# Optimization experiments

Hardware: AMD Instinct MI355X
Metric: run time of the kernel (lower is better)

## Reference

```python
import jax, jax.numpy as jnp
import numpy as np

H, T, E = 8, 2048, 512


def setup_inputs() -> dict:
    key = jax.random.key(0)
    ks = jax.random.split(key, 11)
    s_e = 1.0 / np.sqrt(E)
    s_f = 1.0 / np.sqrt(H * T)
    return {
        "x": jax.random.normal(ks[0], (T, E), jnp.float32),
        "y": jax.random.normal(ks[1], (T, E), jnp.float32),
        "z": jax.random.normal(ks[2], (T, E), jnp.float32),
        "Wq": jax.random.normal(ks[3], (H, E, E), jnp.float32) * s_e,
        "bq": jax.random.normal(ks[4], (H, E), jnp.float32) * s_e,
        "Wk": jax.random.normal(ks[5], (H, E, E), jnp.float32) * s_e,
        "bk": jax.random.normal(ks[6], (H, E), jnp.float32) * s_e,
        "Wv": jax.random.normal(ks[7], (H, E, E), jnp.float32) * s_e,
        "bv": jax.random.normal(ks[8], (H, E), jnp.float32) * s_e,
        "Wf": jax.random.normal(ks[9], (T, H * T), jnp.float32) * s_f,
        "bf": jax.random.normal(ks[10], (T,), jnp.float32) * s_f,
    }


def reference(x, y, z, Wq, bq, Wk, bk, Wv, bv, Wf, bf):
    # Per-head projections: torch Linear is x @ W.T + b, W is [out,in]
    q = jnp.einsum("se,hfe->hsf", x, Wq) + bq[:, None, :]  # [H,T,E]
    k = jnp.einsum("se,hfe->hsf", y, Wk) + bk[:, None, :]
    v = jnp.einsum("se,hfe->hsf", z, Wv) + bv[:, None, :]
    # Scores scaled by sqrt(num query rows) = sqrt(T), as in the source
    scores = jnp.einsum("hsf,htf->hst", q, k) / jnp.sqrt(jnp.asarray(T, x.dtype))
    att = jax.nn.softmax(scores, axis=-1)
    heads_out = jnp.einsum("hst,htf->hsf", att, v)  # [H,T,E]
    concat = heads_out.reshape(H * T, E)  # cat along dim 0
    # finalLinear applied to concat.T: [E, H*T] @ Wf.T -> [E, T], then transpose
    final = (concat.T @ Wf.T + bf).T  # [T, E]
    residual = final + z
    # Manual per-row LayerNorm: (x - mean) / sqrt(std^2 + 1e-4), population std
    mean = jnp.mean(residual, axis=1, keepdims=True)
    var = jnp.var(residual, axis=1, keepdims=True)
    return (residual - mean) / jnp.sqrt(var + 1e-4)
```

## Files before the change

kernel.cpp:

```cpp
#include <hip/hip_runtime.h>
#include <hip/hip_bf16.h>
#include <cstdint>


#define HH 8
#define TT 2048
#define EE 512
#define HT (HH * TT)
#define HE (HH * EE)

typedef __bf16 bf16_t;
typedef __attribute__((ext_vector_type(8))) __bf16 bf16x8;
typedef __attribute__((ext_vector_type(4))) float f32x4;

__device__ __forceinline__ void stage_half(const bf16_t* __restrict__ g, bf16_t* l) {
  __builtin_amdgcn_global_load_lds(
      (const __attribute__((address_space(1))) unsigned int*)g,
      (__attribute__((address_space(3))) unsigned int*)l, 16, 0, 0);
}
__device__ __forceinline__ void stage_half(const float* __restrict__ g, bf16_t* l) {
  float4 u = ((const float4*)g)[0];
  float4 v = ((const float4*)g)[1];
  bf16x8 o;
  o[0] = (__bf16)u.x; o[1] = (__bf16)u.y; o[2] = (__bf16)u.z; o[3] = (__bf16)u.w;
  o[4] = (__bf16)v.x; o[5] = (__bf16)v.y; o[6] = (__bf16)v.z; o[7] = (__bf16)v.w;
  *(bf16x8*)l = o;
}

template <typename AT, typename CT>
__global__ __launch_bounds__(256) void mfma_gemm_nt(
    const AT* __restrict__ A, const bf16_t* __restrict__ B, CT* __restrict__ C,
    const float* __restrict__ bias_m, const float* __restrict__ bias_n,
    int K, int lda, int ldb, int ldc,
    int64_t sA, int64_t sB, int64_t sC, int64_t sBM, int64_t sBN) {
  const int gx = gridDim.x, gy = gridDim.y;
  const int nwg = gx * gy * (int)gridDim.z;
  const int lin = blockIdx.x + gx * (blockIdx.y + gy * blockIdx.z);
  const int qn = nwg >> 3, rn = nwg & 7;
  const int xcd = lin & 7, sub = lin >> 3;
  const int wgid = (xcd < rn ? xcd * (qn + 1) : rn * (qn + 1) + (xcd - rn) * qn) + sub;
  const int bx = wgid % gx;
  const int t1 = wgid / gx;
  const int by = t1 % gy;
  const int z = t1 / gy;

  A += z * sA;
  B += z * sB;
  C += z * sC;
  if (bias_m) bias_m += z * sBM;
  if (bias_n) bias_n += z * sBN;

  const int m0 = bx * 128;
  const int n0 = by * 128;
  const int tid = threadIdx.x;

  __shared__ bf16_t sAb[128 * 32];
  __shared__ bf16_t sBb[128 * 32];

  const int srow = tid >> 2;
  const int scol = (tid & 3) * 8;
  const AT* a0 = A + (int64_t)(m0 + srow) * lda + scol;
  const AT* a1 = a0 + (int64_t)64 * lda;
  const bf16_t* b0 = B + (int64_t)(n0 + srow) * ldb + scol;
  const bf16_t* b1 = b0 + (int64_t)64 * ldb;
  bf16_t* la0 = sAb + tid * 8;
  bf16_t* la1 = sAb + 2048 + tid * 8;
  bf16_t* lb0 = sBb + tid * 8;
  bf16_t* lb1 = sBb + 2048 + tid * 8;

  const int wave = tid >> 6;
  const int lane = tid & 63;
  const int wm = (wave >> 1) * 64;
  const int wn = (wave & 1) * 64;
  const int fr = lane & 15;
  const int qd = lane >> 4;

  f32x4 acc[4][4];
#pragma unroll
  for (int i = 0; i < 4; i++)
#pragma unroll
    for (int j = 0; j < 4; j++) acc[i][j] = (f32x4){0.f, 0.f, 0.f, 0.f};

  for (int kt = 0; kt < K; kt += 32) {
    __syncthreads();
    stage_half(a0 + kt, la0);
    stage_half(a1 + kt, la1);
    stage_half(b0 + kt, lb0);
    stage_half(b1 + kt, lb1);
    __syncthreads();

    bf16x8 af[4], bf_[4];
#pragma unroll
    for (int i = 0; i < 4; i++)
      af[i] = *(const bf16x8*)&sAb[(wm + i * 16 + fr) * 32 + qd * 8];
#pragma unroll
    for (int j = 0; j < 4; j++)
      bf_[j] = *(const bf16x8*)&sBb[(wn + j * 16 + fr) * 32 + qd * 8];
#pragma unroll
    for (int i = 0; i < 4; i++)
#pragma unroll
      for (int j = 0; j < 4; j++)
        acc[i][j] = __builtin_amdgcn_mfma_f32_16x16x32_bf16(af[i], bf_[j], acc[i][j], 0, 0, 0);
  }

#pragma unroll
  for (int i = 0; i < 4; i++) {
    const int row0 = m0 + wm + i * 16 + qd * 4;
#pragma unroll
    for (int j = 0; j < 4; j++) {
      const int col = n0 + wn + j * 16 + fr;
      const float bn = bias_n ? bias_n[col] : 0.f;
#pragma unroll
      for (int r = 0; r < 4; r++) {
        const float bm = bias_m ? bias_m[row0 + r] : 0.f;
        C[(int64_t)(row0 + r) * ldc + col] = (CT)(acc[i][j][r] + bn + bm);
      }
    }
  }
}

__global__ __launch_bounds__(256) void cvt_bf16(const float* __restrict__ s,
                                                bf16_t* __restrict__ d) {
  const int64_t i = ((int64_t)blockIdx.x * 256 + threadIdx.x) * 8;
  float4 u = ((const float4*)(s + i))[0];
  float4 v = ((const float4*)(s + i))[1];
  bf16x8 o;
  o[0] = (__bf16)u.x; o[1] = (__bf16)u.y; o[2] = (__bf16)u.z; o[3] = (__bf16)u.w;
  o[4] = (__bf16)v.x; o[5] = (__bf16)v.y; o[6] = (__bf16)v.z; o[7] = (__bf16)v.w;
  *(bf16x8*)(d + i) = o;
}

__global__ __launch_bounds__(256) void softmax_rows(bf16_t* __restrict__ S) {
  const float scale = 0.022097086912079608f;
  bf16_t* p = S + (int64_t)blockIdx.x * TT;
  const int tid = threadIdx.x;
  bf16x8 in = *(const bf16x8*)(p + tid * 8);
  float v[8];
  float mx = -1e30f;
#pragma unroll
  for (int i = 0; i < 8; i++) {
    v[i] = (float)in[i] * scale;
    mx = fmaxf(mx, v[i]);
  }
#pragma unroll
  for (int o = 32; o > 0; o >>= 1) mx = fmaxf(mx, __shfl_xor(mx, o));
  __shared__ float redm[4], reds[4];
  if ((tid & 63) == 0) redm[tid >> 6] = mx;
  __syncthreads();
  mx = fmaxf(fmaxf(redm[0], redm[1]), fmaxf(redm[2], redm[3]));
  float sum = 0.f;
#pragma unroll
  for (int i = 0; i < 8; i++) {
    v[i] = __expf(v[i] - mx);
    sum += v[i];
  }
#pragma unroll
  for (int o = 32; o > 0; o >>= 1) sum += __shfl_xor(sum, o);
  if ((tid & 63) == 0) reds[tid >> 6] = sum;
  __syncthreads();
  sum = reds[0] + reds[1] + reds[2] + reds[3];
  const float inv = 1.0f / sum;
  bf16x8 o8;
#pragma unroll
  for (int i = 0; i < 8; i++) o8[i] = (__bf16)(v[i] * inv);
  *(bf16x8*)(p + tid * 8) = o8;
}

__global__ __launch_bounds__(256) void ln_res(const float* __restrict__ F,
                                              const float* __restrict__ Z,
                                              const float* __restrict__ BF,
                                              float* __restrict__ O) {
  const int row = blockIdx.x;
  const int tid = threadIdx.x;
  const int64_t off = (int64_t)row * EE + tid;
  float a = 0.f, b = 0.f;
#pragma unroll
  for (int pz = 0; pz < 8; pz++) {
    const float* f = F + (int64_t)pz * TT * EE;
    a += f[off];
    b += f[off + 256];
  }
  const float bft = BF[row];
  a += bft + Z[off];
  b += bft + Z[off + 256];
  float s = a + b, ss = a * a + b * b;
#pragma unroll
  for (int w = 32; w > 0; w >>= 1) {
    s += __shfl_xor(s, w);
    ss += __shfl_xor(ss, w);
  }
  __shared__ float rs[4], rss[4];
  if ((tid & 63) == 0) {
    rs[tid >> 6] = s;
    rss[tid >> 6] = ss;
  }
  __syncthreads();
  s = rs[0] + rs[1] + rs[2] + rs[3];
  ss = rss[0] + rss[1] + rss[2] + rss[3];
  const float mean = s * (1.0f / EE);
  const float var = ss * (1.0f / EE) - mean * mean;
  const float inv = rsqrtf(var + 1e-4f);
  float* o = O + (int64_t)row * EE;
  o[tid] = (a - mean) * inv;
  o[tid + 256] = (b - mean) * inv;
}

extern "C" void kernel_launch(void* const* d_in, const int* in_sizes, int n_in,
                              void* d_out, int out_size, void* d_ws, size_t ws_size,
                              hipStream_t stream) {
  const float* x = (const float*)d_in[0];
  const float* y = (const float*)d_in[1];
  const float* z = (const float*)d_in[2];
  const float* Wq = (const float*)d_in[3];
  const float* bq = (const float*)d_in[4];
  const float* Wk = (const float*)d_in[5];
  const float* bk = (const float*)d_in[6];
  const float* Wv = (const float*)d_in[7];
  const float* bv = (const float*)d_in[8];
  const float* Wf = (const float*)d_in[9];
  const float* bfb = (const float*)d_in[10];
  float* out = (float*)d_out;

  const size_t MB = 1ull << 20;
  char* p = (char*)d_ws;

  const int64_t nTE = (int64_t)TT * EE;
  const int64_t nW = (int64_t)HH * EE * EE;

  if (ws_size >= 151 * MB) {
    bf16_t* xb = (bf16_t*)(p + 0 * MB);
    bf16_t* yb = (bf16_t*)(p + 2 * MB);
    bf16_t* zb = (bf16_t*)(p + 4 * MB);
    bf16_t* Wqb = (bf16_t*)(p + 6 * MB);
    bf16_t* Wkb = (bf16_t*)(p + 10 * MB);
    bf16_t* Wvb = (bf16_t*)(p + 14 * MB);
    bf16_t* q = (bf16_t*)(p + 18 * MB);
    bf16_t* k = (bf16_t*)(p + 34 * MB);
    bf16_t* vT = (bf16_t*)(p + 50 * MB);
    bf16_t* att = (bf16_t*)(p + 66 * MB);
    bf16_t* hoT = (bf16_t*)(p + 130 * MB);
    float* finp = (float*)(p + 18 * MB);

    cvt_bf16<<<nTE / 2048, 256, 0, stream>>>(x, xb);
    cvt_bf16<<<nTE / 2048, 256, 0, stream>>>(y, yb);
    cvt_bf16<<<nTE / 2048, 256, 0, stream>>>(z, zb);
    cvt_bf16<<<nW / 2048, 256, 0, stream>>>(Wq, Wqb);
    cvt_bf16<<<nW / 2048, 256, 0, stream>>>(Wk, Wkb);
    cvt_bf16<<<nW / 2048, 256, 0, stream>>>(Wv, Wvb);

    mfma_gemm_nt<bf16_t, bf16_t><<<dim3(16, 32, 1), 256, 0, stream>>>(
        xb, Wqb, q, nullptr, bq, EE, EE, EE, HE, 0, 0, 0, 0, 0);
    mfma_gemm_nt<bf16_t, bf16_t><<<dim3(16, 32, 1), 256, 0, stream>>>(
        yb, Wkb, k, nullptr, bk, EE, EE, EE, HE, 0, 0, 0, 0, 0);
    mfma_gemm_nt<bf16_t, bf16_t><<<dim3(32, 16, 1), 256, 0, stream>>>(
        Wvb, zb, vT, bv, nullptr, EE, EE, EE, TT, 0, 0, 0, 0, 0);
    mfma_gemm_nt<bf16_t, bf16_t><<<dim3(16, 16, 8), 256, 0, stream>>>(
        q, k, att, nullptr, nullptr, EE, HE, HE, TT, EE, EE, (int64_t)TT * TT, 0, 0);
    softmax_rows<<<HH * TT, 256, 0, stream>>>(att);
    mfma_gemm_nt<bf16_t, bf16_t><<<dim3(4, 16, 8), 256, 0, stream>>>(
        vT, att, hoT, nullptr, nullptr, TT, TT, TT, HT, (int64_t)EE * TT, (int64_t)TT * TT,
        (int64_t)TT, 0, 0);
    mfma_gemm_nt<float, float><<<dim3(16, 4, 8), 256, 0, stream>>>(
        Wf, hoT, finp, nullptr, nullptr, HT / 8, HT, HT, EE, HT / 8, HT / 8,
        (int64_t)TT * EE, 0, 0);
    ln_res<<<TT, 256, 0, stream>>>(finp, z, bfb, out);
  } else {
    bf16_t* xb = (bf16_t*)(p + 0 * MB);
    bf16_t* yb = (bf16_t*)(p + 2 * MB);
    bf16_t* zb = (bf16_t*)(p + 4 * MB);
    bf16_t* Wqb = (bf16_t*)(p + 6 * MB);
    bf16_t* Wkb = (bf16_t*)(p + 10 * MB);
    bf16_t* Wvb = (bf16_t*)(p + 14 * MB);
    bf16_t* qh = (bf16_t*)(p + 18 * MB);
    bf16_t* kh = (bf16_t*)(p + 20 * MB);
    bf16_t* vTh = (bf16_t*)(p + 22 * MB);
    bf16_t* att = (bf16_t*)(p + 24 * MB);
    bf16_t* hoT = (bf16_t*)(p + 32 * MB);
    float* finp = (float*)(p + 0 * MB);

    cvt_bf16<<<nTE / 2048, 256, 0, stream>>>(x, xb);
    cvt_bf16<<<nTE / 2048, 256, 0, stream>>>(y, yb);
    cvt_bf16<<<nTE / 2048, 256, 0, stream>>>(z, zb);
    cvt_bf16<<<nW / 2048, 256, 0, stream>>>(Wq, Wqb);
    cvt_bf16<<<nW / 2048, 256, 0, stream>>>(Wk, Wkb);
    cvt_bf16<<<nW / 2048, 256, 0, stream>>>(Wv, Wvb);

    for (int h = 0; h < HH; h++) {
      const bf16_t* Wq_h = Wqb + (int64_t)h * EE * EE;
      const bf16_t* Wk_h = Wkb + (int64_t)h * EE * EE;
      const bf16_t* Wv_h = Wvb + (int64_t)h * EE * EE;
      mfma_gemm_nt<bf16_t, bf16_t><<<dim3(16, 4, 1), 256, 0, stream>>>(
          xb, Wq_h, qh, nullptr, bq + h * EE, EE, EE, EE, EE, 0, 0, 0, 0, 0);
      mfma_gemm_nt<bf16_t, bf16_t><<<dim3(16, 4, 1), 256, 0, stream>>>(
          yb, Wk_h, kh, nullptr, bk + h * EE, EE, EE, EE, EE, 0, 0, 0, 0, 0);
      mfma_gemm_nt<bf16_t, bf16_t><<<dim3(4, 16, 1), 256, 0, stream>>>(
          Wv_h, zb, vTh, bv + h * EE, nullptr, EE, EE, EE, TT, 0, 0, 0, 0, 0);
      mfma_gemm_nt<bf16_t, bf16_t><<<dim3(16, 16, 1), 256, 0, stream>>>(
          qh, kh, att, nullptr, nullptr, EE, EE, EE, TT, 0, 0, 0, 0, 0);
      softmax_rows<<<TT, 256, 0, stream>>>(att);
      mfma_gemm_nt<bf16_t, bf16_t><<<dim3(4, 16, 1), 256, 0, stream>>>(
          vTh, att, hoT + (int64_t)h * TT, nullptr, nullptr, TT, TT, TT, HT, 0, 0, 0, 0, 0);
    }
    mfma_gemm_nt<float, float><<<dim3(16, 4, 8), 256, 0, stream>>>(
        Wf, hoT, finp, nullptr, nullptr, HT / 8, HT, HT, EE, HT / 8, HT / 8,
        (int64_t)TT * EE, 0, 0);
    ln_res<<<TT, 256, 0, stream>>>(finp, z, bfb, out);
  }
}
```

Baseline: 494.9 us.

## Double-buffer GEMM LDS tiles and raise split-K for final linear

Makes the MFMA GEMM mainloop double-buffered: while one LDS buffer is consumed by MFMAs, the next k-slice is staged asynchronously (global_load_lds for bf16, register prefetch plus convert for fp32 A). This hides global load latency and drops one barrier per k-step. The final Wf GEMM also moves from 8-way to 16-way split-K for more workgroups, and the LayerNorm reducer now sums a runtime count of partials. The finp buffer is relocated to fit the extra partials, at the cost of more partial traffic and double the LDS per block.

```diff
diff --git a/kernel.cpp b/kernel.cpp
--- a/kernel.cpp
+++ b/kernel.cpp
@@ -13,18 +13,17 @@
 typedef __attribute__((ext_vector_type(8))) __bf16 bf16x8;
 typedef __attribute__((ext_vector_type(4))) float f32x4;
 
-__device__ __forceinline__ void stage_half(const bf16_t* __restrict__ g, bf16_t* l) {
+__device__ __forceinline__ void gld_lds16(const bf16_t* __restrict__ g, bf16_t* l) {
   __builtin_amdgcn_global_load_lds(
       (const __attribute__((address_space(1))) unsigned int*)g,
       (__attribute__((address_space(3))) unsigned int*)l, 16, 0, 0);
 }
-__device__ __forceinline__ void stage_half(const float* __restrict__ g, bf16_t* l) {
-  float4 u = ((const float4*)g)[0];
-  float4 v = ((const float4*)g)[1];
+
+__device__ __forceinline__ bf16x8 cvt8(float4 u, float4 v) {
   bf16x8 o;
   o[0] = (__bf16)u.x; o[1] = (__bf16)u.y; o[2] = (__bf16)u.z; o[3] = (__bf16)u.w;
   o[4] = (__bf16)v.x; o[5] = (__bf16)v.y; o[6] = (__bf16)v.z; o[7] = (__bf16)v.w;
-  *(bf16x8*)l = o;
+  return o;
 }
 
 template <typename AT, typename CT>
@@ -54,8 +53,8 @@
   const int n0 = by * 128;
   const int tid = threadIdx.x;
 
-  __shared__ bf16_t sAb[128 * 32];
-  __shared__ bf16_t sBb[128 * 32];
+  __shared__ bf16_t sAb[2][128 * 32];
+  __shared__ bf16_t sBb[2][128 * 32];
 
   const int srow = tid >> 2;
   const int scol = (tid & 3) * 8;
@@ -63,10 +62,6 @@
   const AT* a1 = a0 + (int64_t)64 * lda;
   const bf16_t* b0 = B + (int64_t)(n0 + srow) * ldb + scol;
   const bf16_t* b1 = b0 + (int64_t)64 * ldb;
-  bf16_t* la0 = sAb + tid * 8;
-  bf16_t* la1 = sAb + 2048 + tid * 8;
-  bf16_t* lb0 = sBb + tid * 8;
-  bf16_t* lb1 = sBb + 2048 + tid * 8;
 
   const int wave = tid >> 6;
   const int lane = tid & 63;
@@ -81,27 +76,88 @@
 #pragma unroll
     for (int j = 0; j < 4; j++) acc[i][j] = (f32x4){0.f, 0.f, 0.f, 0.f};
 
-  for (int kt = 0; kt < K; kt += 32) {
+  float4 pa[4];
+
+#define STAGE_B(buf, kt)                              \
+  do {                                                \
+    gld_lds16(b0 + (kt), &sBb[buf][tid * 8]);         \
+    gld_lds16(b1 + (kt), &sBb[buf][2048 + tid * 8]);  \
+  } while (0)
+
+#define STAGE_A_BF16(buf, kt)                         \
+  do {                                                \
+    gld_lds16(a0 + (kt), &sAb[buf][tid * 8]);         \
+    gld_lds16(a1 + (kt), &sAb[buf][2048 + tid * 8]);  \
+  } while (0)
+
+#define LOAD_A_F32(kt)                                \
+  do {                                                \
+    pa[0] = ((const float4*)(a0 + (kt)))[0];          \
+    pa[1] = ((const float4*)(a0 + (kt)))[1];          \
+    pa[2] = ((const float4*)(a1 + (kt)))[0];          \
+    pa[3] = ((const float4*)(a1 + (kt)))[1];          \
+  } while (0)
+
+#define WRITE_A_F32(buf)                                      \
+  do {                                                        \
+    *(bf16x8*)&sAb[buf][tid * 8] = cvt8(pa[0], pa[1]);        \
+    *(bf16x8*)&sAb[buf][2048 + tid * 8] = cvt8(pa[2], pa[3]); \
+  } while (0)
+
+#define COMPUTE(buf)                                                                   \
+  do {                                                                                 \
+    bf16x8 af[4], bf_[4];                                                              \
+    _Pragma("unroll") for (int i = 0; i < 4; i++)                                      \
+        af[i] = *(const bf16x8*)&sAb[buf][(wm + i * 16 + fr) * 32 + qd * 8];           \
+    _Pragma("unroll") for (int j = 0; j < 4; j++)                                      \
+        bf_[j] = *(const bf16x8*)&sBb[buf][(wn + j * 16 + fr) * 32 + qd * 8];          \
+    _Pragma("unroll") for (int i = 0; i < 4; i++)                                      \
+        _Pragma("unroll") for (int j = 0; j < 4; j++)                                  \
+            acc[i][j] =                                                                \
+                __builtin_amdgcn_mfma_f32_16x16x32_bf16(af[i], bf_[j], acc[i][j], 0, 0, 0); \
+  } while (0)
+
+  if constexpr (sizeof(AT) == 2) {
+    STAGE_A_BF16(0, 0);
+  } else {
+    LOAD_A_F32(0);
+    WRITE_A_F32(0);
+  }
+  STAGE_B(0, 0);
+  __syncthreads();
+
+  for (int kt = 0; kt < K; kt += 64) {
+    if constexpr (sizeof(AT) == 2) {
+      STAGE_A_BF16(1, kt + 32);
+    } else {
+      LOAD_A_F32(kt + 32);
+    }
+    STAGE_B(1, kt + 32);
+    COMPUTE(0);
+    if constexpr (sizeof(AT) == 4) WRITE_A_F32(1);
     __syncthreads();
-    stage_half(a0 + kt, la0);
-    stage_half(a1 + kt, la1);
-    stage_half(b0 + kt, lb0);
-    stage_half(b1 + kt, lb1);
+
+    const bool more = (kt + 64) < K;
+    if (more) {
+      if constexpr (sizeof(AT) == 2) {
+        STAGE_A_BF16(0, kt + 64);
+      } else {
+        LOAD_A_F32(kt + 64);
+      }
+      STAGE_B(0, kt + 64);
+    }
+    COMPUTE(1);
+    if constexpr (sizeof(AT) == 4) {
+      if (more) WRITE_A_F32(0);
+    }
     __syncthreads();
-
-    bf16x8 af[4], bf_[4];
-#pragma unroll
-    for (int i = 0; i < 4; i++)
-      af[i] = *(const bf16x8*)&sAb[(wm + i * 16 + fr) * 32 + qd * 8];
-#pragma unroll
-    for (int j = 0; j < 4; j++)
-      bf_[j] = *(const bf16x8*)&sBb[(wn + j * 16 + fr) * 32 + qd * 8];
-#pragma unroll
-    for (int i = 0; i < 4; i++)
-#pragma unroll
-      for (int j = 0; j < 4; j++)
-        acc[i][j] = __builtin_amdgcn_mfma_f32_16x16x32_bf16(af[i], bf_[j], acc[i][j], 0, 0, 0);
-  }
+  }
+
+#undef STAGE_B
+#undef STAGE_A_BF16
+#undef LOAD_A_F32
+#undef WRITE_A_F32
+#undef COMPUTE
 
 #pragma unroll
   for (int i = 0; i < 4; i++) {
@@ -124,10 +180,7 @@
   const int64_t i = ((int64_t)blockIdx.x * 256 + threadIdx.x) * 8;
   float4 u = ((const float4*)(s + i))[0];
   float4 v = ((const float4*)(s + i))[1];
-  bf16x8 o;
-  o[0] = (__bf16)u.x; o[1] = (__bf16)u.y; o[2] = (__bf16)u.z; o[3] = (__bf16)u.w;
-  o[4] = (__bf16)v.x; o[5] = (__bf16)v.y; o[6] = (__bf16)v.z; o[7] = (__bf16)v.w;
-  *(bf16x8*)(d + i) = o;
+  *(bf16x8*)(d + i) = cvt8(u, v);
 }
 
 __global__ __launch_bounds__(256) void softmax_rows(bf16_t* __restrict__ S) {
@@ -169,13 +222,12 @@
 __global__ __launch_bounds__(256) void ln_res(const float* __restrict__ F,
                                               const float* __restrict__ Z,
                                               const float* __restrict__ BF,
-                                              float* __restrict__ O) {
+                                              float* __restrict__ O, int np) {
   const int row = blockIdx.x;
   const int tid = threadIdx.x;
   const int64_t off = (int64_t)row * EE + tid;
   float a = 0.f, b = 0.f;
-#pragma unroll
-  for (int pz = 0; pz < 8; pz++) {
+  for (int pz = 0; pz < np; pz++) {
     const float* f = F + (int64_t)pz * TT * EE;
     a += f[off];
     b += f[off + 256];
@@ -239,7 +291,7 @@
     bf16_t* vT = (bf16_t*)(p + 50 * MB);
     bf16_t* att = (bf16_t*)(p + 66 * MB);
     bf16_t* hoT = (bf16_t*)(p + 130 * MB);
-    float* finp = (float*)(p + 18 * MB);
+    float* finp = (float*)(p + 66 * MB);
 
     cvt_bf16<<<nTE / 2048, 256, 0, stream>>>(x, xb);
     cvt_bf16<<<nTE / 2048, 256, 0, stream>>>(y, yb);
@@ -260,10 +312,10 @@
     mfma_gemm_nt<bf16_t, bf16_t><<<dim3(4, 16, 8), 256, 0, stream>>>(
         vT, att, hoT, nullptr, nullptr, TT, TT, TT, HT, (int64_t)EE * TT, (int64_t)TT * TT,
         (int64_t)TT, 0, 0);
-    mfma_gemm_nt<float, float><<<dim3(16, 4, 8), 256, 0, stream>>>(
-        Wf, hoT, finp, nullptr, nullptr, HT / 8, HT, HT, EE, HT / 8, HT / 8,
+    mfma_gemm_nt<float, float><<<dim3(16, 4, 16), 256, 0, stream>>>(
+        Wf, hoT, finp, nullptr, nullptr, HT / 16, HT, HT, EE, HT / 16, HT / 16,
         (int64_t)TT * EE, 0, 0);
-    ln_res<<<TT, 256, 0, stream>>>(finp, z, bfb, out);
+    ln_res<<<TT, 256, 0, stream>>>(finp, z, bfb, out, 16);
   } else {
     bf16_t* xb = (bf16_t*)(p + 0 * MB);
     bf16_t* yb = (bf16_t*)(p + 2 * MB);
@@ -304,6 +356,6 @@
     mfma_gemm_nt<float, float><<<dim3(16, 4, 8), 256, 0, stream>>>(
         Wf, hoT, finp, nullptr, nullptr, HT / 8, HT, HT, EE, HT / 8, HT / 8,
         (int64_t)TT * EE, 0, 0);
-    ln_res<<<TT, 256, 0, stream>>>(finp, z, bfb, out);
-  }
-}
+    ln_res<<<TT, 256, 0, stream>>>(finp, z, bfb, out, 8);
+  }
+}
```

Result: slower. 509.0 us (+2.9%).
